# Optimization experiments

Measured on AMD Instinct MI355X. Metric: run time of the kernel, lower is better.

The kernel has to match this reference:

```python
import jax, jax.numpy as jnp
import numpy as np

EPS = 1e-7  # keras backend epsilon

def setup_inputs() -> dict:
    key = jax.random.key(0)
    k1, k2, k3 = jax.random.split(key, 3)
    B, L, D, P = 16, 1024, 256, 20
    sent1 = jax.random.normal(k1, (B, L, D), dtype=jnp.float32)
    sent2 = jax.random.normal(k2, (B, L, D), dtype=jnp.float32)
    kernel = jax.random.normal(k3, (P, D), dtype=jnp.float32) * 0.1
    return {"sent1": sent1, "sent2": sent2, "kernel": kernel}

def reference(sent1, sent2, kernel):
    # token norms with keras-style clamping: sqrt(max(sum(x^2), eps))
    n1 = jnp.sqrt(jnp.maximum(jnp.sum(sent1 * sent1, axis=-1), EPS))  # [B,L1]
    n2 = jnp.sqrt(jnp.maximum(jnp.sum(sent2 * sent2, axis=-1), EPS))  # [B,L2]
    # all-pairs cosine matrix via matmul instead of broadcast-multiply-reduce
    dots = jnp.einsum('bld,bmd->blm', sent1, sent2)                    # [B,L1,L2]
    cos = dots / n1[:, :, None] / n2[:, None, :]
    # mean attentive vectors: cosine-weighted sum of sent2, normalized by row sum
    weighted = jnp.einsum('blm,bmd->bld', cos, sent2)                  # [B,L1,D]
    mav = weighted / (jnp.sum(cos, axis=-1, keepdims=True) + EPS)      # [B,L1,D]
    # perspective-weighted cosine between sent1*k and mav*k, fused without [B,L,P,D]
    k2 = kernel * kernel                                               # [P,D]
    num = jnp.einsum('bld,pd->blp', sent1 * mav, k2)                   # sum_d s1*mav*k^2
    nv1 = jnp.sqrt(jnp.maximum(jnp.einsum('bld,pd->blp', sent1 * sent1, k2), EPS))
    nv2 = jnp.sqrt(jnp.maximum(jnp.einsum('bld,pd->blp', mav * mav, k2), EPS))
    return num / nv1 / nv2                                             # [B,L1,P]
```

## Files before the change

kernel.cpp:

```cpp
#include <hip/hip_runtime.h>
#include <math.h>

#define EPS 1e-7f

constexpr int B = 16, L = 1024, D = 256, P = 20;
constexpr int LD = L * D;
constexpr int DD = D * D;

typedef __attribute__((ext_vector_type(8))) _Float16 f16x8;
typedef __attribute__((ext_vector_type(4))) float f32x4;


__device__ inline unsigned short f2h(float x) {
    _Float16 h = (_Float16)x;
    union { _Float16 h; unsigned short u; } c; c.h = h; return c.u;
}
__device__ inline float h2f(unsigned short u) {
    union { unsigned short u; _Float16 h; } c; c.u = u; return (float)c.h;
}

__global__ __launch_bounds__(512) void k_prep2(const float* __restrict__ s2,
                                               float* __restrict__ tp,
                                               unsigned short* __restrict__ CT) {
    __shared__ float tile[32][260];
    __shared__ float wiv[32];
    __shared__ float wsq[32];
    __shared__ float tpp[2][256];
    int tid = threadIdx.x;
    int b   = blockIdx.x >> 5, mt = blockIdx.x & 31;
    int m0  = mt * 32;
    const float* gbase = s2 + (size_t)b * LD + (size_t)m0 * D;
    float4 v[4];
#pragma unroll
    for (int i = 0; i < 4; ++i) {
        int u = tid + i * 512;
        v[i] = *(const float4*)(gbase + (size_t)(u >> 6) * D + (u & 63) * 4);
    }
#pragma unroll
    for (int i = 0; i < 4; ++i) {
        int u = tid + i * 512;
        *(float4*)&tile[u >> 6][(u & 63) * 4] = v[i];
    }
    __syncthreads();
    {
        int r = tid >> 4, seg = tid & 15;
        float s = 0.f;
#pragma unroll
        for (int q = 0; q < 4; ++q) {
            float4 x = *(const float4*)&tile[r][seg * 16 + q * 4];
            s += x.x * x.x + x.y * x.y + x.z * x.z + x.w * x.w;
        }
#pragma unroll
        for (int o = 8; o; o >>= 1) s += __shfl_down(s, o, 16);
        if (seg == 0) {
            float iv = 1.0f / sqrtf(fmaxf(s, EPS));
            wiv[r] = iv;
            wsq[r] = sqrtf(iv);
        }
    }
    __syncthreads();
    {
        int dc = tid & 255, h = tid >> 8;
        float tpart = 0.f;
#pragma unroll
        for (int mm = 0; mm < 16; ++mm) {
            int m = h * 16 + mm;
            tpart += tile[m][dc] * wiv[m];
        }
        tpp[h][dc] = tpart;
    }
    {
        unsigned short* cbase = CT + (size_t)b * LD + m0;
#pragma unroll
        for (int i = 0; i < 2; ++i) {
            int u = tid + i * 512;
            int d = u >> 2, c = u & 3;
            union { unsigned short us[8]; uint4 q; } pk;
#pragma unroll
            for (int k = 0; k < 8; ++k) {
                int m = c * 8 + k;
                pk.us[k] = f2h(tile[m][d] * wsq[m]);
            }
            *(uint4*)(cbase + (size_t)d * L + c * 8) = pk.q;
        }
    }
    __syncthreads();
    if (tid < 256)
        tp[(size_t)(mt * B + b) * D + tid] = tpp[0][tid] + tpp[1][tid];
}

__global__ __launch_bounds__(256) void k_gram32(const unsigned short* __restrict__ CT,
                                                unsigned short* __restrict__ Gf) {
    __shared__ short smem[2 * 32 * 264];
    short* As = smem;
    short* Bs = smem + 32 * 264;
    int tid = threadIdx.x;
    int b   = blockIdx.x / 36;
    int t   = blockIdx.x - b * 36;
    int ti = 0, rem = t;
    while (rem >= 8 - ti) { rem -= 8 - ti; ++ti; }
    int tj = ti + rem;
    bool diag = (ti == tj);
    int wave = tid >> 6, lane = tid & 63;
    int lr = lane & 15, lq = lane >> 4;

    const unsigned short* rowA = CT + (size_t)b * LD + (size_t)(ti * 32) * L;
    const unsigned short* rowB = CT + (size_t)b * LD + (size_t)(tj * 32) * L;

    f32x4 acc[2][2];
#pragma unroll
    for (int i = 0; i < 2; ++i)
#pragma unroll
        for (int j = 0; j < 2; ++j) acc[i][j] = (f32x4){0.f, 0.f, 0.f, 0.f};

#pragma unroll 1
    for (int kb = 0; kb < 4; ++kb) {
        int koff = kb * 256;
        __syncthreads();
        {
#pragma unroll
            for (int i = 0; i < 4; ++i) {
                int u = tid + i * 256;
                int row = u >> 5, c = u & 31;
                *(uint4*)&As[row * 264 + c * 8] =
                    *(const uint4*)(rowA + (size_t)row * L + koff + c * 8);
            }
            if (!diag) {
#pragma unroll
                for (int i = 0; i < 4; ++i) {
                    int u = tid + i * 256;
                    int row = u >> 5, c = u & 31;
                    *(uint4*)&Bs[row * 264 + c * 8] =
                        *(const uint4*)(rowB + (size_t)row * L + koff + c * 8);
                }
            }
        }
        __syncthreads();
        const short* Bp = diag ? As : Bs;
#pragma unroll
        for (int kk = 0; kk < 2; ++kk) {
            int ks = wave * 2 + kk;
            f16x8 af[2], bf[2];
#pragma unroll
            for (int i = 0; i < 2; ++i)
                af[i] = *(const f16x8*)&As[(i * 16 + lr) * 264 + ks * 32 + lq * 8];
#pragma unroll
            for (int j = 0; j < 2; ++j)
                bf[j] = *(const f16x8*)&Bp[(j * 16 + lr) * 264 + ks * 32 + lq * 8];
#pragma unroll
            for (int i = 0; i < 2; ++i)
#pragma unroll
                for (int j = 0; j < 2; ++j)
                    acc[i][j] = __builtin_amdgcn_mfma_f32_16x16x32_f16(af[i], bf[j], acc[i][j], 0, 0, 0);
        }
    }
    __syncthreads();
    float* red = (float*)smem;
#pragma unroll
    for (int i = 0; i < 2; ++i)
#pragma unroll
        for (int j = 0; j < 2; ++j)
#pragma unroll
            for (int r = 0; r < 4; ++r) {
                int row = i * 16 + lq * 4 + r, col = j * 16 + lr;
                red[wave * 1056 + row * 33 + col] = acc[i][j][r];
            }
    __syncthreads();
    unsigned short* gout = Gf + (size_t)b * DD;
#pragma unroll
    for (int k = 0; k < 4; ++k) {
        int e = tid + k * 256;
        int row = e >> 5, col = e & 31;
        float s = red[row * 33 + col] + red[1056 + row * 33 + col] +
                  red[2112 + row * 33 + col] + red[3168 + row * 33 + col];
        gout[(size_t)(ti * 32 + row) * D + tj * 32 + col] = f2h(s);
    }
    if (!diag) {
#pragma unroll
        for (int k = 0; k < 4; ++k) {
            int e = tid + k * 256;
            int r2 = e >> 5, c2 = e & 31;
            float s = red[c2 * 33 + r2] + red[1056 + c2 * 33 + r2] +
                      red[2112 + c2 * 33 + r2] + red[3168 + c2 * 33 + r2];
            gout[(size_t)(tj * 32 + r2) * D + ti * 32 + c2] = f2h(s);
        }
    }
}

__global__ __launch_bounds__(256) void k_mav_out(const float* __restrict__ s1,
                                                 const float* __restrict__ tp,
                                                 const unsigned short* __restrict__ Gf,
                                                 const float* __restrict__ kern,
                                                 float* __restrict__ out) {
    __shared__ short As[16 * 264];
    __shared__ short Ms[16 * 264];
    __shared__ float k2s[P * 264];
    __shared__ float ts[256];
    __shared__ float sgnS[16];
    int tid  = threadIdx.x;
    int b    = blockIdx.x >> 6, lt = blockIdx.x & 63;
    int l0   = lt * 16;
    int wave = tid >> 6, lane = tid & 63;
    int lr   = lane & 15, lq = lane >> 4;

    float4 sv[4];
    const float* s1b = s1 + (size_t)(b * L + l0) * D;
#pragma unroll
    for (int i = 0; i < 4; ++i) {
        int u = tid + i * 256;
        sv[i] = *(const float4*)(s1b + (size_t)(u >> 6) * D + (u & 63) * 4);
    }

    {
        float a = 0.f;
#pragma unroll
        for (int mc = 0; mc < 32; ++mc) a += tp[(size_t)(mc * B + b) * D + tid];
        ts[tid] = a;
    }
#pragma unroll
    for (int p = 0; p < P; ++p) {
        float v = kern[p * D + tid];
        k2s[p * 264 + tid] = v * v;
    }
    __syncthreads();

    {
        float up[4], sq[4];
#pragma unroll
        for (int i = 0; i < 4; ++i) {
            int u = tid + i * 256;
            int c = u & 63;
            float4 x = sv[i];
            float4 tv = *(const float4*)(ts + c * 4);
            up[i] = x.x * tv.x + x.y * tv.y + x.z * tv.z + x.w * tv.w;
            sq[i] = x.x * x.x + x.y * x.y + x.z * x.z + x.w * x.w;
            ushort4 h4;
            h4.x = f2h(x.x); h4.y = f2h(x.y); h4.z = f2h(x.z); h4.w = f2h(x.w);
            *(ushort4*)&As[(u >> 6) * 264 + c * 4] = h4;
        }
#pragma unroll
        for (int i = 0; i < 4; ++i) {
#pragma unroll
            for (int o = 32; o; o >>= 1) {
                up[i] += __shfl_down(up[i], o, 64);
                sq[i] += __shfl_down(sq[i], o, 64);
            }
            if (lane == 0) {
                float n1v = sqrtf(fmaxf(sq[i], EPS));
                sgnS[wave + 4 * i] = up[i] + EPS * n1v;
            }
        }
    }
    __syncthreads();

    {
        int n0 = wave * 64;
        f16x8 af[8];
#pragma unroll
        for (int ks = 0; ks < 8; ++ks)
            af[ks] = *(const f16x8*)&As[lr * 264 + ks * 32 + lq * 8];
        const unsigned short* gb0 = Gf + (size_t)b * DD + (size_t)(n0 + lr) * D + lq * 8;
#pragma unroll 2
        for (int j = 0; j < 4; ++j) {
            const unsigned short* gb = gb0 + (size_t)(j * 16) * D;
            f32x4 acc = (f32x4){0.f, 0.f, 0.f, 0.f};
#pragma unroll
            for (int ks = 0; ks < 8; ++ks) {
                f16x8 bf = *(const f16x8*)(gb + ks * 32);
                acc = __builtin_amdgcn_mfma_f32_16x16x32_f16(af[ks], bf, acc, 0, 0, 0);
            }
#pragma unroll
            for (int r4 = 0; r4 < 4; ++r4)
                Ms[(lq * 4 + r4) * 264 + n0 + j * 16 + lr] = f2h(acc[r4]);
        }
    }
    __syncthreads();

    int dg = lane & 15, ps = lane >> 4;
#pragma unroll 1
    for (int rl = 0; rl < 4; ++rl) {
        int l = wave * 4 + rl;
        float4 sm[4], ss[4], mm[4];
#pragma unroll
        for (int j = 0; j < 4; ++j) {
            ushort4 h4 = *(const ushort4*)&As[l * 264 + dg * 4 + j * 64];
            ushort4 m4 = *(const ushort4*)&Ms[l * 264 + dg * 4 + j * 64];
            float4 sx, mx;
            sx.x = h2f(h4.x); sx.y = h2f(h4.y); sx.z = h2f(h4.z); sx.w = h2f(h4.w);
            mx.x = h2f(m4.x); mx.y = h2f(m4.y); mx.z = h2f(m4.z); mx.w = h2f(m4.w);
            sm[j].x = sx.x * mx.x; sm[j].y = sx.y * mx.y; sm[j].z = sx.z * mx.z; sm[j].w = sx.w * mx.w;
            ss[j].x = sx.x * sx.x; ss[j].y = sx.y * sx.y; ss[j].z = sx.z * sx.z; ss[j].w = sx.w * sx.w;
            mm[j].x = mx.x * mx.x; mm[j].y = mx.y * mx.y; mm[j].z = mx.z * mx.z; mm[j].w = mx.w * mx.w;
        }
        float sgn = (sgnS[l] < 0.f) ? -1.f : 1.f;
#pragma unroll
        for (int tI = 0; tI < 5; ++tI) {
            int p = ps + tI * 4;
            float na = 0.f, nb = 0.f, nc = 0.f;
#pragma unroll
            for (int j = 0; j < 4; ++j) {
                float4 kv = *(const float4*)&k2s[p * 264 + j * 64 + dg * 4];
                na += sm[j].x * kv.x + sm[j].y * kv.y + sm[j].z * kv.z + sm[j].w * kv.w;
                nb += ss[j].x * kv.x + ss[j].y * kv.y + ss[j].z * kv.z + ss[j].w * kv.w;
                nc += mm[j].x * kv.x + mm[j].y * kv.y + mm[j].z * kv.z + mm[j].w * kv.w;
            }
#pragma unroll
            for (int o = 8; o; o >>= 1) {
                na += __shfl_down(na, o, 16);
                nb += __shfl_down(nb, o, 16);
                nc += __shfl_down(nc, o, 16);
            }
            if (dg == 0) {
                out[(size_t)(b * L + l0 + l) * P + p] =
                    sgn * na * rsqrtf(fmaxf(nb, EPS)) * rsqrtf(fmaxf(nc, EPS));
            }
        }
    }
}

extern "C" void kernel_launch(void* const* d_in, const int* in_sizes, int n_in,
                              void* d_out, int out_size, void* d_ws, size_t ws_size,
                              hipStream_t stream) {
    const float* s1   = (const float*)d_in[0];
    const float* s2   = (const float*)d_in[1];
    const float* kern = (const float*)d_in[2];
    float* out = (float*)d_out;
    float* ws  = (float*)d_ws;

    float* tp = ws;
    unsigned short* CT = (unsigned short*)(ws + 131072);
    unsigned short* Gf = (unsigned short*)(ws + 2228224);

    k_prep2<<<512, 512, 0, stream>>>(s2, tp, CT);
    k_gram32<<<576, 256, 0, stream>>>(CT, Gf);
    k_mav_out<<<1024, 256, 0, stream>>>(s1, tp, Gf, kern, out);
}
```

Baseline: 124.2 us.

## Use MFMA for perspective reductions and double row tile in mav_out

The final kernel now handles 32 rows per block instead of 16, which halves the grid and the per-block reloads of tp and the kernel weights. The three perspective reductions (s1*mav, s1^2, mav^2 against k^2) move from scalar FMA loops with shuffle reductions to fp16 MFMA against a padded fp16 k^2 tile. The mav values are scaled down before fp16 storage to avoid overflow when squared. The cost is precision: the products and squares are now formed in fp16, which risks overflow or accuracy loss.

```diff
diff --git a/kernel.cpp b/kernel.cpp
--- a/kernel.cpp
+++ b/kernel.cpp
@@ -10,6 +10,8 @@
 typedef __attribute__((ext_vector_type(8))) _Float16 f16x8;
 typedef __attribute__((ext_vector_type(4))) float f32x4;
 
+
+#define MAV_SCALE 0.00390625f
 
 __device__ inline unsigned short f2h(float x) {
     _Float16 h = (_Float16)x;
@@ -192,25 +194,17 @@
                                                  const unsigned short* __restrict__ Gf,
                                                  const float* __restrict__ kern,
                                                  float* __restrict__ out) {
-    __shared__ short As[16 * 264];
-    __shared__ short Ms[16 * 264];
-    __shared__ float k2s[P * 264];
+    __shared__ short As[32 * 264];
+    __shared__ short Ms[32 * 264];
+    __shared__ short k2h[32 * 264];
     __shared__ float ts[256];
-    __shared__ float sgnS[16];
+    __shared__ float sgnS[32];
     int tid  = threadIdx.x;
-    int b    = blockIdx.x >> 6, lt = blockIdx.x & 63;
-    int l0   = lt * 16;
+    int b    = blockIdx.x >> 5, lt = blockIdx.x & 31;
+    int l0   = lt * 32;
     int wave = tid >> 6, lane = tid & 63;
     int lr   = lane & 15, lq = lane >> 4;
 
-    float4 sv[4];
-    const float* s1b = s1 + (size_t)(b * L + l0) * D;
-#pragma unroll
-    for (int i = 0; i < 4; ++i) {
-        int u = tid + i * 256;
-        sv[i] = *(const float4*)(s1b + (size_t)(u >> 6) * D + (u & 63) * 4);
-    }
-
     {
         float a = 0.f;
 #pragma unroll
@@ -218,50 +212,52 @@
         ts[tid] = a;
     }
 #pragma unroll
-    for (int p = 0; p < P; ++p) {
-        float v = kern[p * D + tid];
-        k2s[p * 264 + tid] = v * v;
-    }
-    __syncthreads();
-
-    {
-        float up[4], sq[4];
-#pragma unroll
-        for (int i = 0; i < 4; ++i) {
-            int u = tid + i * 256;
-            int c = u & 63;
-            float4 x = sv[i];
-            float4 tv = *(const float4*)(ts + c * 4);
-            up[i] = x.x * tv.x + x.y * tv.y + x.z * tv.z + x.w * tv.w;
-            sq[i] = x.x * x.x + x.y * x.y + x.z * x.z + x.w * x.w;
-            ushort4 h4;
-            h4.x = f2h(x.x); h4.y = f2h(x.y); h4.z = f2h(x.z); h4.w = f2h(x.w);
-            *(ushort4*)&As[(u >> 6) * 264 + c * 4] = h4;
-        }
-#pragma unroll
-        for (int i = 0; i < 4; ++i) {
-#pragma unroll
-            for (int o = 32; o; o >>= 1) {
-                up[i] += __shfl_down(up[i], o, 64);
-                sq[i] += __shfl_down(sq[i], o, 64);
-            }
-            if (lane == 0) {
-                float n1v = sqrtf(fmaxf(sq[i], EPS));
-                sgnS[wave + 4 * i] = up[i] + EPS * n1v;
-            }
-        }
-    }
-    __syncthreads();
-
-    {
-        int n0 = wave * 64;
+    for (int p = 0; p < 32; ++p) {
+        unsigned short hv = 0;
+        if (p < P) {
+            float v = kern[p * D + tid];
+            hv = f2h(v * v);
+        }
+        k2h[p * 264 + tid] = hv;
+    }
+    __syncthreads();
+
+    {
+        int r = tid >> 3, seg = tid & 7;
+        const float* gp = s1 + (size_t)(b * L + l0 + r) * D + seg * 32;
+        float up = 0.f, sq = 0.f;
+        union { unsigned short us[32]; uint4 q[4]; } hb;
+#pragma unroll
+        for (int q8 = 0; q8 < 8; ++q8) {
+            float4 v = ((const float4*)gp)[q8];
+            int td = seg * 32 + q8 * 4;
+            up += v.x * ts[td] + v.y * ts[td + 1] + v.z * ts[td + 2] + v.w * ts[td + 3];
+            sq += v.x * v.x + v.y * v.y + v.z * v.z + v.w * v.w;
+            hb.us[q8 * 4 + 0] = f2h(v.x); hb.us[q8 * 4 + 1] = f2h(v.y);
+            hb.us[q8 * 4 + 2] = f2h(v.z); hb.us[q8 * 4 + 3] = f2h(v.w);
+        }
+        short* la = &As[r * 264 + seg * 32];
+        ((uint4*)la)[0] = hb.q[0]; ((uint4*)la)[1] = hb.q[1];
+        ((uint4*)la)[2] = hb.q[2]; ((uint4*)la)[3] = hb.q[3];
+#pragma unroll
+        for (int o = 4; o; o >>= 1) { up += __shfl_down(up, o, 8); sq += __shfl_down(sq, o, 8); }
+        if (seg == 0) {
+            float n1v = sqrtf(fmaxf(sq, EPS));
+            sgnS[r] = up + EPS * n1v;
+        }
+    }
+    __syncthreads();
+
+    {
+        int rowg = wave & 1;
+        int c0   = (wave >> 1) * 128;
         f16x8 af[8];
 #pragma unroll
         for (int ks = 0; ks < 8; ++ks)
-            af[ks] = *(const f16x8*)&As[lr * 264 + ks * 32 + lq * 8];
-        const unsigned short* gb0 = Gf + (size_t)b * DD + (size_t)(n0 + lr) * D + lq * 8;
+            af[ks] = *(const f16x8*)&As[(rowg * 16 + lr) * 264 + ks * 32 + lq * 8];
+        const unsigned short* gb0 = Gf + (size_t)b * DD + (size_t)(c0 + lr) * D + lq * 8;
 #pragma unroll 2
-        for (int j = 0; j < 4; ++j) {
+        for (int j = 0; j < 8; ++j) {
             const unsigned short* gb = gb0 + (size_t)(j * 16) * D;
             f32x4 acc = (f32x4){0.f, 0.f, 0.f, 0.f};
 #pragma unroll
@@ -271,48 +267,38 @@
             }
 #pragma unroll
             for (int r4 = 0; r4 < 4; ++r4)
-                Ms[(lq * 4 + r4) * 264 + n0 + j * 16 + lr] = f2h(acc[r4]);
-        }
-    }
-    __syncthreads();
-
-    int dg = lane & 15, ps = lane >> 4;
-#pragma unroll 1
-    for (int rl = 0; rl < 4; ++rl) {
-        int l = wave * 4 + rl;
-        float4 sm[4], ss[4], mm[4];
-#pragma unroll
-        for (int j = 0; j < 4; ++j) {
-            ushort4 h4 = *(const ushort4*)&As[l * 264 + dg * 4 + j * 64];
-            ushort4 m4 = *(const ushort4*)&Ms[l * 264 + dg * 4 + j * 64];
-            float4 sx, mx;
-            sx.x = h2f(h4.x); sx.y = h2f(h4.y); sx.z = h2f(h4.z); sx.w = h2f(h4.w);
-            mx.x = h2f(m4.x); mx.y = h2f(m4.y); mx.z = h2f(m4.z); mx.w = h2f(m4.w);
-            sm[j].x = sx.x * mx.x; sm[j].y = sx.y * mx.y; sm[j].z = sx.z * mx.z; sm[j].w = sx.w * mx.w;
-            ss[j].x = sx.x * sx.x; ss[j].y = sx.y * sx.y; ss[j].z = sx.z * sx.z; ss[j].w = sx.w * sx.w;
-            mm[j].x = mx.x * mx.x; mm[j].y = mx.y * mx.y; mm[j].z = mx.z * mx.z; mm[j].w = mx.w * mx.w;
-        }
-        float sgn = (sgnS[l] < 0.f) ? -1.f : 1.f;
-#pragma unroll
-        for (int tI = 0; tI < 5; ++tI) {
-            int p = ps + tI * 4;
-            float na = 0.f, nb = 0.f, nc = 0.f;
-#pragma unroll
-            for (int j = 0; j < 4; ++j) {
-                float4 kv = *(const float4*)&k2s[p * 264 + j * 64 + dg * 4];
-                na += sm[j].x * kv.x + sm[j].y * kv.y + sm[j].z * kv.z + sm[j].w * kv.w;
-                nb += ss[j].x * kv.x + ss[j].y * kv.y + ss[j].z * kv.z + ss[j].w * kv.w;
-                nc += mm[j].x * kv.x + mm[j].y * kv.y + mm[j].z * kv.z + mm[j].w * kv.w;
-            }
-#pragma unroll
-            for (int o = 8; o; o >>= 1) {
-                na += __shfl_down(na, o, 16);
-                nb += __shfl_down(nb, o, 16);
-                nc += __shfl_down(nc, o, 16);
-            }
-            if (dg == 0) {
-                out[(size_t)(b * L + l0 + l) * P + p] =
-                    sgn * na * rsqrtf(fmaxf(nb, EPS)) * rsqrtf(fmaxf(nc, EPS));
+                Ms[(rowg * 16 + lq * 4 + r4) * 264 + c0 + j * 16 + lr] =
+                    f2h(acc[r4] * MAV_SCALE);
+        }
+    }
+    __syncthreads();
+
+    {
+        int rowg = wave & 1;
+        int pt   = wave >> 1;
+        f32x4 ax = (f32x4){0.f, 0.f, 0.f, 0.f};
+        f32x4 an = (f32x4){0.f, 0.f, 0.f, 0.f};
+        f32x4 am = (f32x4){0.f, 0.f, 0.f, 0.f};
+#pragma unroll
+        for (int ks = 0; ks < 8; ++ks) {
+            f16x8 sa = *(const f16x8*)&As[(rowg * 16 + lr) * 264 + ks * 32 + lq * 8];
+            f16x8 ma = *(const f16x8*)&Ms[(rowg * 16 + lr) * 264 + ks * 32 + lq * 8];
+            f16x8 bf = *(const f16x8*)&k2h[(pt * 16 + lr) * 264 + ks * 32 + lq * 8];
+            f16x8 xa = sa * ma;
+            f16x8 s2 = sa * sa;
+            f16x8 m2 = ma * ma;
+            ax = __builtin_amdgcn_mfma_f32_16x16x32_f16(xa, bf, ax, 0, 0, 0);
+            an = __builtin_amdgcn_mfma_f32_16x16x32_f16(s2, bf, an, 0, 0, 0);
+            am = __builtin_amdgcn_mfma_f32_16x16x32_f16(m2, bf, am, 0, 0, 0);
+        }
+        int p = pt * 16 + lr;
+        if (p < P) {
+#pragma unroll
+            for (int r4 = 0; r4 < 4; ++r4) {
+                int row = rowg * 16 + lq * 4 + r4;
+                float sgn = (sgnS[row] < 0.f) ? -1.f : 1.f;
+                out[(size_t)(b * L + l0 + row) * P + p] =
+                    sgn * ax[r4] * rsqrtf(fmaxf(an[r4], EPS)) * rsqrtf(fmaxf(am[r4], EPS));
             }
         }
     }
@@ -333,5 +319,5 @@
 
     k_prep2<<<512, 512, 0, stream>>>(s2, tp, CT);
     k_gram32<<<576, 256, 0, stream>>>(CT, Gf);
-    k_mav_out<<<1024, 256, 0, stream>>>(s1, tp, Gf, kern, out);
-}
+    k_mav_out<<<512, 256, 0, stream>>>(s1, tp, Gf, kern, out);
+}
```

New measurement: 109.3 us. 12.0% less time.
